# Performance work log

Measured on AMD Instinct MI355X. Metric: run time of the kernel, lower is better.

## Reference

```python
import jax, jax.numpy as jnp
import numpy as np

IN, H, B, T, OUT = 128, 512, 256, 512, 2

def _lstm_layer(x, Wih, Whh, bih, bhh):
    # x: [B, T, D_in] -> h_seq: [B, T, H]. PyTorch gate order: i, f, g, o.
    gx = jnp.einsum('btd,gd->btg', x, Wih) + bih + bhh  # [B, T, 4H]
    gx = jnp.transpose(gx, (1, 0, 2))                    # [T, B, 4H]
    Hh = Whh.shape[1]
    def step(carry, g_t):
        h, c = carry
        g = g_t + h @ Whh.T
        i = jax.nn.sigmoid(g[:, 0*Hh:1*Hh])
        f = jax.nn.sigmoid(g[:, 1*Hh:2*Hh])
        gg = jnp.tanh(g[:, 2*Hh:3*Hh])
        o = jax.nn.sigmoid(g[:, 3*Hh:4*Hh])
        c = f * c + i * gg
        h = o * jnp.tanh(c)
        return (h, c), h
    h0 = jnp.zeros((x.shape[0], Hh), x.dtype)
    (_, _), hs = jax.lax.scan(step, (h0, h0), gx)
    return jnp.transpose(hs, (1, 0, 2))  # [B, T, H]

def setup_inputs() -> dict:
    key = jax.random.key(0)
    ks = jax.random.split(key, 11)
    s = 1.0 / np.sqrt(H)
    u = lambda k, shp: jax.random.uniform(k, shp, jnp.float32, -s, s)
    return {
        'x':    jax.random.normal(ks[0], (B, T, IN), jnp.float32),
        'Wih0': u(ks[1], (4 * H, IN)), 'Whh0': u(ks[2], (4 * H, H)),
        'bih0': u(ks[3], (4 * H,)),    'bhh0': u(ks[4], (4 * H,)),
        'Wih1': u(ks[5], (4 * H, H)),  'Whh1': u(ks[6], (4 * H, H)),
        'bih1': u(ks[7], (4 * H,)),    'bhh1': u(ks[8], (4 * H,)),
        'Wfc':  u(ks[9], (OUT, H)),    'bfc':  u(ks[10], (OUT,)),
    }

def reference(x, Wih0, Whh0, bih0, bhh0, Wih1, Whh1, bih1, bhh1, Wfc, bfc):
    h1 = _lstm_layer(x, Wih0, Whh0, bih0, bhh0)   # layer 0
    h2 = _lstm_layer(h1, Wih1, Whh1, bih1, bhh1)  # layer 1
    return h2[:, -1, :] @ Wfc.T + bfc             # [B, OUT]
```

## Files before the change

### kernel.cpp

```cpp
#include <hip/hip_runtime.h>

#define IN_DIM 128
#define HID    512
#define BATCH  256
#define SEQT   512
#define G4H    2048
#define K0     640
#define K1     1024
#define NC0    20
#define NC1    32
#define ROWB   2048
#define FSTRIDE 32

typedef __attribute__((ext_vector_type(8))) short bf16x8;
typedef __attribute__((ext_vector_type(4))) float f32x4;

#define MFMA16 __builtin_amdgcn_mfma_f32_16x16x32_bf16
#define GL(r, g, c) ((r) * 132 + (g) * 33 + (c))

__device__ __forceinline__ unsigned short f2bf(float f) {
  unsigned u = __float_as_uint(f);
  u += 0x7fffu + ((u >> 16) & 1u);
  return (unsigned short)(u >> 16);
}
__device__ __forceinline__ float bf2f(unsigned short s) {
  return __uint_as_float(((unsigned)s) << 16);
}
__device__ __forceinline__ float sigm(float x) { return 1.0f / (1.0f + __expf(-x)); }
__device__ __forceinline__ float tanh_f(float x) {
  float xc = fminf(fmaxf(x, -15.0f), 15.0f);
  float e = __expf(2.0f * xc);
  return (e - 1.0f) / (e + 1.0f);
}

__device__ __forceinline__ unsigned ald(const unsigned* p) {
  return __hip_atomic_load(p, __ATOMIC_RELAXED, __HIP_MEMORY_SCOPE_AGENT);
}

__global__ void conv_weights(const float* __restrict__ Wih0, const float* __restrict__ Whh0,
                             const float* __restrict__ Wih1, const float* __restrict__ Whh1,
                             const float* __restrict__ bih0, const float* __restrict__ bhh0,
                             const float* __restrict__ bih1, const float* __restrict__ bhh1,
                             short* __restrict__ W0h, short* __restrict__ W0l,
                             short* __restrict__ W1h, short* __restrict__ W1l,
                             float* __restrict__ bsum0, float* __restrict__ bsum1) {
  int idx = blockIdx.x * blockDim.x + threadIdx.x;
  const int N0 = G4H * K0, N1 = G4H * K1;
  if (idx < N0) {
    int tile = idx / (K0 * 16), rem = idx % (K0 * 16);
    int kcg = rem >> 9, l = (rem >> 3) & 63, j = rem & 7;
    int slice = tile >> 2, g = tile & 3;
    int c = l & 15, k = kcg * 32 + ((l >> 4) << 3) + j;
    int n = g * HID + slice * 16 + c;
    float w = (k < IN_DIM) ? Wih0[n * IN_DIM + k] : Whh0[n * HID + (k - IN_DIM)];
    unsigned short hi = f2bf(w);
    W0h[idx] = (short)hi;
    W0l[idx] = (short)f2bf(w - bf2f(hi));
  } else if (idx < N0 + N1) {
    int d = idx - N0;
    int tile = d / (K1 * 16), rem = d % (K1 * 16);
    int kcg = rem >> 9, l = (rem >> 3) & 63, j = rem & 7;
    int slice = tile >> 2, g = tile & 3;
    int c = l & 15, k = kcg * 32 + ((l >> 4) << 3) + j;
    int n = g * HID + slice * 16 + c;
    float w = (k < HID) ? Wih1[n * HID + k] : Whh1[n * HID + (k - HID)];
    unsigned short hi = f2bf(w);
    W1h[d] = (short)hi;
    W1l[d] = (short)f2bf(w - bf2f(hi));
  } else if (idx < N0 + N1 + G4H) {
    int n = idx - (N0 + N1);
    bsum0[n] = bih0[n] + bhh0[n];
  } else if (idx < N0 + N1 + 2 * G4H) {
    int n = idx - (N0 + N1 + G4H);
    bsum1[n] = bih1[n] + bhh1[n];
  }
}

#define PKH(a, b) ((unsigned)((a) & 0xffffu) | (((b) & 0xffffu) << 16))
#define PKL(a, b) (((a) >> 16) | ((b) & 0xffff0000u))

__device__ __forceinline__ void unpack16(char* bh, char* bl, int byte0, int rx,
                                         const uint4& v0, const uint4& v1,
                                         const uint4& v2, const uint4& v3) {
  int4 h0 = {(int)PKH(v0.x, v0.y), (int)PKH(v0.z, v0.w), (int)PKH(v1.x, v1.y), (int)PKH(v1.z, v1.w)};
  int4 h1 = {(int)PKH(v2.x, v2.y), (int)PKH(v2.z, v2.w), (int)PKH(v3.x, v3.y), (int)PKH(v3.z, v3.w)};
  int4 l0 = {(int)PKL(v0.x, v0.y), (int)PKL(v0.z, v0.w), (int)PKL(v1.x, v1.y), (int)PKL(v1.z, v1.w)};
  int4 l1 = {(int)PKL(v2.x, v2.y), (int)PKL(v2.z, v2.w), (int)PKL(v3.x, v3.y), (int)PKL(v3.z, v3.w)};
  *(int4*)(bh + (byte0 ^ rx)) = h0;
  *(int4*)(bh + ((byte0 + 16) ^ rx)) = h1;
  *(int4*)(bl + (byte0 ^ rx)) = l0;
  *(int4*)(bl + ((byte0 + 16) ^ rx)) = l1;
}

__device__ __forceinline__ void stage_one(char* AhiB, char* AloB,
                                          const unsigned* __restrict__ plane,
                                          int b0, int colOff, int tid) {
  const int row = tid >> 5, c32 = tid & 31;
  const unsigned* p = plane + (size_t)(b0 + row) * HID + c32 * 16;
  uint4 v0, v1, v2, v3;
  asm volatile(
      "global_load_dwordx4 %0, %4, off sc0 sc1\n\t"
      "global_load_dwordx4 %1, %4, off offset:16 sc0 sc1\n\t"
      "global_load_dwordx4 %2, %4, off offset:32 sc0 sc1\n\t"
      "global_load_dwordx4 %3, %4, off offset:48 sc0 sc1\n\t"
      "s_waitcnt vmcnt(0)"
      : "=&v"(v0), "=&v"(v1), "=&v"(v2), "=&v"(v3)
      : "v"(p)
      : "memory");
  const int rx = (row & 7) << 4;
  unpack16(AhiB + row * ROWB, AloB + row * ROWB, (colOff + c32 * 16) * 2, rx, v0, v1, v2, v3);
}

__device__ __forceinline__ void stage_two(char* AhiB, char* AloB,
                                          const unsigned* __restrict__ pA,
                                          const unsigned* __restrict__ pB,
                                          int b0, int tid) {
  const int row = tid >> 5, c32 = tid & 31;
  const unsigned* p0 = pA + (size_t)(b0 + row) * HID + c32 * 16;
  const unsigned* p2 = pB + (size_t)(b0 + row) * HID + c32 * 16;
  uint4 v0, v1, v2, v3, w0, w1, w2, w3;
  asm volatile(
      "global_load_dwordx4 %0, %8, off sc0 sc1\n\t"
      "global_load_dwordx4 %1, %8, off offset:16 sc0 sc1\n\t"
      "global_load_dwordx4 %2, %8, off offset:32 sc0 sc1\n\t"
      "global_load_dwordx4 %3, %8, off offset:48 sc0 sc1\n\t"
      "global_load_dwordx4 %4, %9, off sc0 sc1\n\t"
      "global_load_dwordx4 %5, %9, off offset:16 sc0 sc1\n\t"
      "global_load_dwordx4 %6, %9, off offset:32 sc0 sc1\n\t"
      "global_load_dwordx4 %7, %9, off offset:48 sc0 sc1\n\t"
      "s_waitcnt vmcnt(0)"
      : "=&v"(v0), "=&v"(v1), "=&v"(v2), "=&v"(v3),
        "=&v"(w0), "=&v"(w1), "=&v"(w2), "=&v"(w3)
      : "v"(p0), "v"(p2)
      : "memory");
  const int rx = (row & 7) << 4;
  char* bh = AhiB + row * ROWB;
  char* bl = AloB + row * ROWB;
  unpack16(bh, bl, (c32 * 16) * 2, rx, v0, v1, v2, v3);
  unpack16(bh, bl, (HID + c32 * 16) * 2, rx, w0, w1, w2, w3);
}
#undef PKH
#undef PKL

template <int NKC>
__device__ __forceinline__ void gemm32(const char* Ah, const char* Al,
                                       const short* __restrict__ Bh0, const short* __restrict__ Bl0,
                                       const short* __restrict__ Bh1, const short* __restrict__ Bl1,
                                       int lane, int aoff,
                                       f32x4& a00, f32x4& a01, f32x4& a10, f32x4& a11) {
  const int row = lane & 15;
  const int ko  = (lane >> 4) * 8;
  const int rx  = (row & 7) << 4;
  const char* pAh0 = Ah + row * ROWB;
  const char* pAh1 = Ah + (row + 16) * ROWB;
  const char* pAl0 = Al + row * ROWB;
  const char* pAl1 = Al + (row + 16) * ROWB;
#pragma unroll
  for (int kc = 0; kc < NKC; ++kc) {
    const int off = ((aoff + kc * 32 + ko) * 2) ^ rx;
    bf16x8 ah0 = *(const bf16x8*)(pAh0 + off);
    bf16x8 ah1 = *(const bf16x8*)(pAh1 + off);
    bf16x8 al0 = *(const bf16x8*)(pAl0 + off);
    bf16x8 al1 = *(const bf16x8*)(pAl1 + off);
    bf16x8 bh0 = *(const bf16x8*)(Bh0 + kc * 512 + lane * 8);
    bf16x8 bl0 = *(const bf16x8*)(Bl0 + kc * 512 + lane * 8);
    bf16x8 bh1 = *(const bf16x8*)(Bh1 + kc * 512 + lane * 8);
    bf16x8 bl1 = *(const bf16x8*)(Bl1 + kc * 512 + lane * 8);
    a00 = MFMA16(ah0, bh0, a00, 0, 0, 0);
    a01 = MFMA16(ah1, bh0, a01, 0, 0, 0);
    a00 = MFMA16(ah0, bl0, a00, 0, 0, 0);
    a01 = MFMA16(ah1, bl0, a01, 0, 0, 0);
    a00 = MFMA16(al0, bh0, a00, 0, 0, 0);
    a01 = MFMA16(al1, bh0, a01, 0, 0, 0);
    a10 = MFMA16(ah0, bh1, a10, 0, 0, 0);
    a11 = MFMA16(ah1, bh1, a11, 0, 0, 0);
    a10 = MFMA16(ah0, bl1, a10, 0, 0, 0);
    a11 = MFMA16(ah1, bl1, a11, 0, 0, 0);
    a10 = MFMA16(al0, bh1, a10, 0, 0, 0);
    a11 = MFMA16(al1, bh1, a11, 0, 0, 0);
  }
}

__device__ __forceinline__ void finq32(float* glf, int g, int lane,
                                       const f32x4& a00, const f32x4& a01,
                                       const f32x4& a10, const f32x4& a11) {
  const int col = lane & 15;
  const int r0  = (lane >> 4) * 4;
#pragma unroll
  for (int r = 0; r < 4; ++r) {
    atomicAdd(glf + GL(r0 + r, g, col), a00[r]);
    atomicAdd(glf + GL(16 + r0 + r, g, col), a01[r]);
    atomicAdd(glf + GL(r0 + r, g, col + 16), a10[r]);
    atomicAdd(glf + GL(16 + r0 + r, g, col + 16), a11[r]);
  }
}

__device__ __forceinline__ void group_barrier(unsigned* flags, unsigned target,
                                              int tid, int wid) {
  asm volatile("s_waitcnt vmcnt(0)" ::: "memory");
  __syncthreads();
  if (tid < 64) {
    if (tid == 0)
      __hip_atomic_store(flags + wid * FSTRIDE, target,
                         __ATOMIC_RELAXED, __HIP_MEMORY_SCOPE_AGENT);
    const int i = (tid & 31) * FSTRIDE;
    while (true) {
      unsigned v = ald(flags + i);
      if (__all((int)(v >= target))) break;
      __builtin_amdgcn_s_sleep(1);
    }
  }
  __syncthreads();
}

__global__ void __launch_bounds__(1024, 4) lstm_fused(
    const float* __restrict__ x,
    const float* __restrict__ Wfc, const float* __restrict__ bfc,
    const short* __restrict__ W0h, const short* __restrict__ W0l,
    const short* __restrict__ W1h, const short* __restrict__ W1l,
    const float* __restrict__ bsum0, const float* __restrict__ bsum1,
    unsigned* __restrict__ h0s, unsigned* __restrict__ h2s,
    unsigned* __restrict__ counters,
    float* __restrict__ out) {
  const int tid  = threadIdx.x;
  const int wv   = tid >> 6;
  const int lane = tid & 63;
  const int wid  = blockIdx.x & 31;
  const int grp  = blockIdx.x >> 5;
  const int role = wid >> 4;
  const int w16  = wid & 15;
  const int hid0 = w16 * 32;
  const int b0   = grp * 32;
  unsigned* flags = counters + grp * (32 * FSTRIDE);

  __shared__ __align__(16) char AhiB[32 * ROWB];
  __shared__ __align__(16) char AloB[32 * ROWB];
  __shared__ float glf[32 * 132];

  const int g  = wv & 3;
  const int kq = wv >> 2;
  const int t0 = (w16 * 2) * 4 + g, t1 = t0 + 4;
  const short *Bh0, *Bl0, *Bh1, *Bl1;
  int aoff;
  if (role == 0) {
    Bh0 = W0h + ((size_t)t0 * NC0 + (size_t)kq * 5) * 512;
    Bl0 = W0l + ((size_t)t0 * NC0 + (size_t)kq * 5) * 512;
    Bh1 = W0h + ((size_t)t1 * NC0 + (size_t)kq * 5) * 512;
    Bl1 = W0l + ((size_t)t1 * NC0 + (size_t)kq * 5) * 512;
    aoff = kq * 160;
  } else {
    Bh0 = W1h + ((size_t)t0 * NC1 + (size_t)kq * 8) * 512;
    Bl0 = W1l + ((size_t)t0 * NC1 + (size_t)kq * 8) * 512;
    Bh1 = W1h + ((size_t)t1 * NC1 + (size_t)kq * 8) * 512;
    Bl1 = W1l + ((size_t)t1 * NC1 + (size_t)kq * 8) * 512;
    aoff = kq * 256;
  }

  float c = 0.f;
  float bs[4];
  {
    const int n = hid0 + (tid & 31);
    const float* bsp = role ? bsum1 : bsum0;
#pragma unroll
    for (int q = 0; q < 4; ++q) bs[q] = bsp[q * HID + n];
  }
  for (int i = tid; i < 32 * 132; i += 1024) glf[i] = 0.f;

  const size_t PL = (size_t)BATCH * HID;

  for (int s = 0; s <= SEQT; ++s) {
    const int cur = s & 1, prv = cur ^ 1;
    unsigned* h0c = h0s + (size_t)cur * PL;
    const unsigned* h0p = h0s + (size_t)prv * PL;
    unsigned* h2c = h2s + (size_t)cur * PL;
    const unsigned* h2p = h2s + (size_t)prv * PL;
    const bool active = role ? (s > 0) : (s < SEQT);

    if (active) {
      if (role == 0) {
        {
          const int row = tid >> 5, t32 = tid & 31;
          const int rx = (row & 7) << 4;
          const float* xs = x + ((size_t)(b0 + row) * SEQT + s) * IN_DIM + t32 * 4;
          float4 xv = *(const float4*)xs;
          unsigned short h0v = f2bf(xv.x), h1v = f2bf(xv.y), h2v = f2bf(xv.z), h3v = f2bf(xv.w);
          uint2 hd = {(unsigned)h0v | ((unsigned)h1v << 16), (unsigned)h2v | ((unsigned)h3v << 16)};
          uint2 ld = {(unsigned)f2bf(xv.x - bf2f(h0v)) | ((unsigned)f2bf(xv.y - bf2f(h1v)) << 16),
                      (unsigned)f2bf(xv.z - bf2f(h2v)) | ((unsigned)f2bf(xv.w - bf2f(h3v)) << 16)};
          const int byte = (t32 * 8) ^ rx;
          *(uint2*)(AhiB + row * ROWB + byte) = hd;
          *(uint2*)(AloB + row * ROWB + byte) = ld;
        }
        stage_one(AhiB, AloB, h0p, b0, IN_DIM, tid);
      } else {
        stage_two(AhiB, AloB, h0p, h2p, b0, tid);
      }
    }
    __syncthreads();

    if (active) {
      f32x4 a00 = {0.f, 0.f, 0.f, 0.f}, a01 = {0.f, 0.f, 0.f, 0.f};
      f32x4 a10 = {0.f, 0.f, 0.f, 0.f}, a11 = {0.f, 0.f, 0.f, 0.f};
      if (role == 0)
        gemm32<5>(AhiB, AloB, Bh0, Bl0, Bh1, Bl1, lane, aoff, a00, a01, a10, a11);
      else
        gemm32<8>(AhiB, AloB, Bh0, Bl0, Bh1, Bl1, lane, aoff, a00, a01, a10, a11);
      finq32(glf, g, lane, a00, a01, a10, a11);
    }
    __syncthreads();

    if (active) {
      const int row = tid >> 5, col = tid & 31;
      float gi = glf[GL(row, 0, col)] + bs[0];
      float gf = glf[GL(row, 1, col)] + bs[1];
      float gg = glf[GL(row, 2, col)] + bs[2];
      float go = glf[GL(row, 3, col)] + bs[3];
      glf[GL(row, 0, col)] = 0.f; glf[GL(row, 1, col)] = 0.f;
      glf[GL(row, 2, col)] = 0.f; glf[GL(row, 3, col)] = 0.f;
      float i = sigm(gi), f = sigm(gf), gv = tanh_f(gg), o = sigm(go);
      float cc = f * c + i * gv;
      c = cc;
      float h = o * tanh_f(cc);
      unsigned short hh = f2bf(h);
      unsigned short hl = f2bf(h - bf2f(hh));
      unsigned pk = (unsigned)hh | ((unsigned)hl << 16);
      unsigned* hc = role ? h2c : h0c;
      __hip_atomic_store(hc + (size_t)(b0 + row) * HID + hid0 + col, pk,
                         __ATOMIC_RELAXED, __HIP_MEMORY_SCOPE_AGENT);
    }

    group_barrier(flags, (unsigned)(s + 1), tid, wid);
  }

  {
    const int p = tid >> 3, q = tid & 7;
    float acc = 0.f;
    if (wid == 0 && tid < 512) {
      const int b = b0 + (p >> 1), o = p & 1;
      const unsigned* sp = h2s + (size_t)b * HID + q * 64;
      const float* wf = Wfc + (size_t)o * HID + q * 64;
#pragma unroll 8
      for (int i = 0; i < 64; ++i) {
        unsigned u = ald(sp + i);
        acc += (bf2f((unsigned short)(u & 0xffff)) + bf2f((unsigned short)(u >> 16))) * wf[i];
      }
      glf[p * 8 + q] = acc;
    }
    __syncthreads();
    if (wid == 0 && tid < 512 && q == 0) {
      float t = 0.f;
#pragma unroll
      for (int i = 0; i < 8; ++i) t += glf[p * 8 + i];
      out[(b0 + (p >> 1)) * 2 + (p & 1)] = t + bfc[p & 1];
    }
  }
}

extern "C" void kernel_launch(void* const* d_in, const int* in_sizes, int n_in,
                              void* d_out, int out_size, void* d_ws, size_t ws_size,
                              hipStream_t stream) {
  const float* x    = (const float*)d_in[0];
  const float* Wih0 = (const float*)d_in[1];
  const float* Whh0 = (const float*)d_in[2];
  const float* bih0 = (const float*)d_in[3];
  const float* bhh0 = (const float*)d_in[4];
  const float* Wih1 = (const float*)d_in[5];
  const float* Whh1 = (const float*)d_in[6];
  const float* bih1 = (const float*)d_in[7];
  const float* bhh1 = (const float*)d_in[8];
  const float* Wfc  = (const float*)d_in[9];
  const float* bfc  = (const float*)d_in[10];
  float* out = (float*)d_out;

  short* W0h = (short*)d_ws;
  short* W0l = W0h + (size_t)G4H * K0;
  short* W1h = W0l + (size_t)G4H * K0;
  short* W1l = W1h + (size_t)G4H * K1;
  unsigned* h0s = (unsigned*)(W1l + (size_t)G4H * K1);
  unsigned* h2s = h0s + (size_t)2 * BATCH * HID;
  unsigned* counters = h2s + (size_t)2 * BATCH * HID;
  float* bsum0 = (float*)(counters + 8 * 32 * FSTRIDE);
  float* bsum1 = bsum0 + G4H;

  (void)hipMemsetAsync(h0s, 0,
                       (size_t)4 * BATCH * HID * sizeof(unsigned) +
                           (size_t)8 * 32 * FSTRIDE * sizeof(unsigned),
                       stream);

  const int total = G4H * K0 + G4H * K1 + 2 * G4H;
  conv_weights<<<(total + 255) / 256, 256, 0, stream>>>(
      Wih0, Whh0, Wih1, Whh1, bih0, bhh0, bih1, bhh1,
      W0h, W0l, W1h, W1l, bsum0, bsum1);

  void* args[] = {(void*)&x,    (void*)&Wfc,  (void*)&bfc,
                  (void*)&W0h,  (void*)&W0l,  (void*)&W1h, (void*)&W1l,
                  (void*)&bsum0, (void*)&bsum1,
                  (void*)&h0s,  (void*)&h2s,  (void*)&counters, (void*)&out};
  (void)hipLaunchCooperativeKernel((void*)lstm_fused, dim3(256), dim3(1024), args, 0,
                                   stream);
}
```

Measured before the change: 16.71 ms.

## Store LSTM hidden state as single bf16 and drop its low-part MFMAs

The hidden states exchanged between workgroups are now stored as one bf16 value instead of a packed hi/lo bf16 pair. This halves the global traffic for the hidden state and the LDS staging buffer, and removes the low-part A-operand MFMAs for the recurrent terms. Only the x input still gets hi/lo splitting, which is applied for the first IN_DIM columns of layer 0. The cost is lower precision in the recurrent matmuls, which could increase error over 512 timesteps.

```diff
diff --git a/kernel.cpp b/kernel.cpp
--- a/kernel.cpp
+++ b/kernel.cpp
@@ -76,92 +76,80 @@
   }
 }
 
-#define PKH(a, b) ((unsigned)((a) & 0xffffu) | (((b) & 0xffffu) << 16))
-#define PKL(a, b) (((a) >> 16) | ((b) & 0xffff0000u))
-
-__device__ __forceinline__ void unpack16(char* bh, char* bl, int byte0, int rx,
-                                         const uint4& v0, const uint4& v1,
-                                         const uint4& v2, const uint4& v3) {
-  int4 h0 = {(int)PKH(v0.x, v0.y), (int)PKH(v0.z, v0.w), (int)PKH(v1.x, v1.y), (int)PKH(v1.z, v1.w)};
-  int4 h1 = {(int)PKH(v2.x, v2.y), (int)PKH(v2.z, v2.w), (int)PKH(v3.x, v3.y), (int)PKH(v3.z, v3.w)};
-  int4 l0 = {(int)PKL(v0.x, v0.y), (int)PKL(v0.z, v0.w), (int)PKL(v1.x, v1.y), (int)PKL(v1.z, v1.w)};
-  int4 l1 = {(int)PKL(v2.x, v2.y), (int)PKL(v2.z, v2.w), (int)PKL(v3.x, v3.y), (int)PKL(v3.z, v3.w)};
-  *(int4*)(bh + (byte0 ^ rx)) = h0;
-  *(int4*)(bh + ((byte0 + 16) ^ rx)) = h1;
-  *(int4*)(bl + (byte0 ^ rx)) = l0;
-  *(int4*)(bl + ((byte0 + 16) ^ rx)) = l1;
-}
-
-__device__ __forceinline__ void stage_one(char* AhiB, char* AloB,
-                                          const unsigned* __restrict__ plane,
-                                          int b0, int colOff, int tid) {
+
+__device__ __forceinline__ void stage_l0(char* Ah, const float* __restrict__ x,
+                                         const unsigned short* __restrict__ h0p,
+                                         int b0, int s, int tid) {
   const int row = tid >> 5, c32 = tid & 31;
-  const unsigned* p = plane + (size_t)(b0 + row) * HID + c32 * 16;
-  uint4 v0, v1, v2, v3;
+  const int rx = (row & 7) << 4;
+  char* base = Ah + row * ROWB;
+  {
+    const float* xs = x + ((size_t)(b0 + row) * SEQT + s) * IN_DIM + c32 * 4;
+    float4 xv = *(const float4*)xs;
+    unsigned short h0 = f2bf(xv.x), h1 = f2bf(xv.y), h2 = f2bf(xv.z), h3 = f2bf(xv.w);
+    uint2 hd = {(unsigned)h0 | ((unsigned)h1 << 16), (unsigned)h2 | ((unsigned)h3 << 16)};
+    uint2 ld = {(unsigned)f2bf(xv.x - bf2f(h0)) | ((unsigned)f2bf(xv.y - bf2f(h1)) << 16),
+                (unsigned)f2bf(xv.z - bf2f(h2)) | ((unsigned)f2bf(xv.w - bf2f(h3)) << 16)};
+    *(uint2*)(base + ((c32 * 8) ^ rx)) = hd;
+    *(uint2*)(base + ((1280 + c32 * 8) ^ rx)) = ld;
+  }
+  {
+    const unsigned short* hp = h0p + (size_t)(b0 + row) * HID + c32 * 16;
+    uint4 v0, v1;
+    asm volatile(
+        "global_load_dwordx4 %0, %2, off sc0 sc1\n\t"
+        "global_load_dwordx4 %1, %2, off offset:16 sc0 sc1\n\t"
+        "s_waitcnt vmcnt(0)"
+        : "=&v"(v0), "=&v"(v1) : "v"(hp) : "memory");
+    const int byte0 = 256 + c32 * 32;
+    *(int4*)(base + (byte0 ^ rx)) = *(int4*)&v0;
+    *(int4*)(base + ((byte0 + 16) ^ rx)) = *(int4*)&v1;
+  }
+}
+
+__device__ __forceinline__ void stage_l1(char* Ah,
+                                         const unsigned short* __restrict__ h0p,
+                                         const unsigned short* __restrict__ h2p,
+                                         int b0, int tid) {
+  const int row = tid >> 5, c32 = tid & 31;
+  const int rx = (row & 7) << 4;
+  char* base = Ah + row * ROWB;
+  const unsigned short* p0 = h0p + (size_t)(b0 + row) * HID + c32 * 16;
+  const unsigned short* p2 = h2p + (size_t)(b0 + row) * HID + c32 * 16;
+  uint4 v0, v1, w0, w1;
   asm volatile(
       "global_load_dwordx4 %0, %4, off sc0 sc1\n\t"
       "global_load_dwordx4 %1, %4, off offset:16 sc0 sc1\n\t"
-      "global_load_dwordx4 %2, %4, off offset:32 sc0 sc1\n\t"
-      "global_load_dwordx4 %3, %4, off offset:48 sc0 sc1\n\t"
+      "global_load_dwordx4 %2, %5, off sc0 sc1\n\t"
+      "global_load_dwordx4 %3, %5, off offset:16 sc0 sc1\n\t"
       "s_waitcnt vmcnt(0)"
-      : "=&v"(v0), "=&v"(v1), "=&v"(v2), "=&v"(v3)
-      : "v"(p)
-      : "memory");
-  const int rx = (row & 7) << 4;
-  unpack16(AhiB + row * ROWB, AloB + row * ROWB, (colOff + c32 * 16) * 2, rx, v0, v1, v2, v3);
-}
-
-__device__ __forceinline__ void stage_two(char* AhiB, char* AloB,
-                                          const unsigned* __restrict__ pA,
-                                          const unsigned* __restrict__ pB,
-                                          int b0, int tid) {
-  const int row = tid >> 5, c32 = tid & 31;
-  const unsigned* p0 = pA + (size_t)(b0 + row) * HID + c32 * 16;
-  const unsigned* p2 = pB + (size_t)(b0 + row) * HID + c32 * 16;
-  uint4 v0, v1, v2, v3, w0, w1, w2, w3;
-  asm volatile(
-      "global_load_dwordx4 %0, %8, off sc0 sc1\n\t"
-      "global_load_dwordx4 %1, %8, off offset:16 sc0 sc1\n\t"
-      "global_load_dwordx4 %2, %8, off offset:32 sc0 sc1\n\t"
-      "global_load_dwordx4 %3, %8, off offset:48 sc0 sc1\n\t"
-      "global_load_dwordx4 %4, %9, off sc0 sc1\n\t"
-      "global_load_dwordx4 %5, %9, off offset:16 sc0 sc1\n\t"
-      "global_load_dwordx4 %6, %9, off offset:32 sc0 sc1\n\t"
-      "global_load_dwordx4 %7, %9, off offset:48 sc0 sc1\n\t"
-      "s_waitcnt vmcnt(0)"
-      : "=&v"(v0), "=&v"(v1), "=&v"(v2), "=&v"(v3),
-        "=&v"(w0), "=&v"(w1), "=&v"(w2), "=&v"(w3)
-      : "v"(p0), "v"(p2)
-      : "memory");
-  const int rx = (row & 7) << 4;
-  char* bh = AhiB + row * ROWB;
-  char* bl = AloB + row * ROWB;
-  unpack16(bh, bl, (c32 * 16) * 2, rx, v0, v1, v2, v3);
-  unpack16(bh, bl, (HID + c32 * 16) * 2, rx, w0, w1, w2, w3);
-}
-#undef PKH
-#undef PKL
+      : "=&v"(v0), "=&v"(v1), "=&v"(w0), "=&v"(w1)
+      : "v"(p0), "v"(p2) : "memory");
+  const int b0b = c32 * 32;
+  *(int4*)(base + (b0b ^ rx)) = *(int4*)&v0;
+  *(int4*)(base + ((b0b + 16) ^ rx)) = *(int4*)&v1;
+  const int b2b = 1024 + c32 * 32;
+  *(int4*)(base + (b2b ^ rx)) = *(int4*)&w0;
+  *(int4*)(base + ((b2b + 16) ^ rx)) = *(int4*)&w1;
+}
 
 template <int NKC>
-__device__ __forceinline__ void gemm32(const char* Ah, const char* Al,
-                                       const short* __restrict__ Bh0, const short* __restrict__ Bl0,
-                                       const short* __restrict__ Bh1, const short* __restrict__ Bl1,
-                                       int lane, int aoff,
-                                       f32x4& a00, f32x4& a01, f32x4& a10, f32x4& a11) {
+__device__ __forceinline__ void gemm_seq(const char* Ah, bool xlo,
+                                         const short* __restrict__ Bh0, const short* __restrict__ Bl0,
+                                         const short* __restrict__ Bh1, const short* __restrict__ Bl1,
+                                         int lane, int aoff,
+                                         f32x4& a00, f32x4& a01, f32x4& a10, f32x4& a11) {
   const int row = lane & 15;
   const int ko  = (lane >> 4) * 8;
   const int rx  = (row & 7) << 4;
-  const char* pAh0 = Ah + row * ROWB;
-  const char* pAh1 = Ah + (row + 16) * ROWB;
-  const char* pAl0 = Al + row * ROWB;
-  const char* pAl1 = Al + (row + 16) * ROWB;
+  const char* pA0 = Ah + row * ROWB;
+  const char* pA1 = Ah + (row + 16) * ROWB;
 #pragma unroll
   for (int kc = 0; kc < NKC; ++kc) {
-    const int off = ((aoff + kc * 32 + ko) * 2) ^ rx;
-    bf16x8 ah0 = *(const bf16x8*)(pAh0 + off);
-    bf16x8 ah1 = *(const bf16x8*)(pAh1 + off);
-    bf16x8 al0 = *(const bf16x8*)(pAl0 + off);
-    bf16x8 al1 = *(const bf16x8*)(pAl1 + off);
+    const int k = aoff + kc * 32;
+    const int off = ((k + ko) * 2) ^ rx;
+    bf16x8 ah0 = *(const bf16x8*)(pA0 + off);
+    bf16x8 ah1 = *(const bf16x8*)(pA1 + off);
     bf16x8 bh0 = *(const bf16x8*)(Bh0 + kc * 512 + lane * 8);
     bf16x8 bl0 = *(const bf16x8*)(Bl0 + kc * 512 + lane * 8);
     bf16x8 bh1 = *(const bf16x8*)(Bh1 + kc * 512 + lane * 8);
@@ -170,14 +158,19 @@
     a01 = MFMA16(ah1, bh0, a01, 0, 0, 0);
     a00 = MFMA16(ah0, bl0, a00, 0, 0, 0);
     a01 = MFMA16(ah1, bl0, a01, 0, 0, 0);
-    a00 = MFMA16(al0, bh0, a00, 0, 0, 0);
-    a01 = MFMA16(al1, bh0, a01, 0, 0, 0);
     a10 = MFMA16(ah0, bh1, a10, 0, 0, 0);
     a11 = MFMA16(ah1, bh1, a11, 0, 0, 0);
     a10 = MFMA16(ah0, bl1, a10, 0, 0, 0);
     a11 = MFMA16(ah1, bl1, a11, 0, 0, 0);
-    a10 = MFMA16(al0, bh1, a10, 0, 0, 0);
-    a11 = MFMA16(al1, bh1, a11, 0, 0, 0);
+    if (xlo && k < IN_DIM) {
+      const int offl = ((1280 + (k + ko) * 2)) ^ rx;
+      bf16x8 al0 = *(const bf16x8*)(pA0 + offl);
+      bf16x8 al1 = *(const bf16x8*)(pA1 + offl);
+      a00 = MFMA16(al0, bh0, a00, 0, 0, 0);
+      a01 = MFMA16(al1, bh0, a01, 0, 0, 0);
+      a10 = MFMA16(al0, bh1, a10, 0, 0, 0);
+      a11 = MFMA16(al1, bh1, a11, 0, 0, 0);
+    }
   }
 }
 
@@ -219,7 +212,7 @@
     const short* __restrict__ W0h, const short* __restrict__ W0l,
     const short* __restrict__ W1h, const short* __restrict__ W1l,
     const float* __restrict__ bsum0, const float* __restrict__ bsum1,
-    unsigned* __restrict__ h0s, unsigned* __restrict__ h2s,
+    unsigned short* __restrict__ h0s, unsigned short* __restrict__ h2s,
     unsigned* __restrict__ counters,
     float* __restrict__ out) {
   const int tid  = threadIdx.x;
@@ -233,8 +226,7 @@
   const int b0   = grp * 32;
   unsigned* flags = counters + grp * (32 * FSTRIDE);
 
-  __shared__ __align__(16) char AhiB[32 * ROWB];
-  __shared__ __align__(16) char AloB[32 * ROWB];
+  __shared__ __align__(16) char AhB[32 * ROWB];
   __shared__ float glf[32 * 132];
 
   const int g  = wv & 3;
@@ -270,31 +262,15 @@
 
   for (int s = 0; s <= SEQT; ++s) {
     const int cur = s & 1, prv = cur ^ 1;
-    unsigned* h0c = h0s + (size_t)cur * PL;
-    const unsigned* h0p = h0s + (size_t)prv * PL;
-    unsigned* h2c = h2s + (size_t)cur * PL;
-    const unsigned* h2p = h2s + (size_t)prv * PL;
+    unsigned short* h0c = h0s + (size_t)cur * PL;
+    const unsigned short* h0p = h0s + (size_t)prv * PL;
+    unsigned short* h2c = h2s + (size_t)cur * PL;
+    const unsigned short* h2p = h2s + (size_t)prv * PL;
     const bool active = role ? (s > 0) : (s < SEQT);
 
     if (active) {
-      if (role == 0) {
-        {
-          const int row = tid >> 5, t32 = tid & 31;
-          const int rx = (row & 7) << 4;
-          const float* xs = x + ((size_t)(b0 + row) * SEQT + s) * IN_DIM + t32 * 4;
-          float4 xv = *(const float4*)xs;
-          unsigned short h0v = f2bf(xv.x), h1v = f2bf(xv.y), h2v = f2bf(xv.z), h3v = f2bf(xv.w);
-          uint2 hd = {(unsigned)h0v | ((unsigned)h1v << 16), (unsigned)h2v | ((unsigned)h3v << 16)};
-          uint2 ld = {(unsigned)f2bf(xv.x - bf2f(h0v)) | ((unsigned)f2bf(xv.y - bf2f(h1v)) << 16),
-                      (unsigned)f2bf(xv.z - bf2f(h2v)) | ((unsigned)f2bf(xv.w - bf2f(h3v)) << 16)};
-          const int byte = (t32 * 8) ^ rx;
-          *(uint2*)(AhiB + row * ROWB + byte) = hd;
-          *(uint2*)(AloB + row * ROWB + byte) = ld;
-        }
-        stage_one(AhiB, AloB, h0p, b0, IN_DIM, tid);
-      } else {
-        stage_two(AhiB, AloB, h0p, h2p, b0, tid);
-      }
+      if (role == 0) stage_l0(AhB, x, h0p, b0, s, tid);
+      else           stage_l1(AhB, h0p, h2p, b0, tid);
     }
     __syncthreads();
 
@@ -302,9 +278,9 @@
       f32x4 a00 = {0.f, 0.f, 0.f, 0.f}, a01 = {0.f, 0.f, 0.f, 0.f};
       f32x4 a10 = {0.f, 0.f, 0.f, 0.f}, a11 = {0.f, 0.f, 0.f, 0.f};
       if (role == 0)
-        gemm32<5>(AhiB, AloB, Bh0, Bl0, Bh1, Bl1, lane, aoff, a00, a01, a10, a11);
+        gemm_seq<5>(AhB, true, Bh0, Bl0, Bh1, Bl1, lane, aoff, a00, a01, a10, a11);
       else
-        gemm32<8>(AhiB, AloB, Bh0, Bl0, Bh1, Bl1, lane, aoff, a00, a01, a10, a11);
+        gemm_seq<8>(AhB, false, Bh0, Bl0, Bh1, Bl1, lane, aoff, a00, a01, a10, a11);
       finq32(glf, g, lane, a00, a01, a10, a11);
     }
     __syncthreads();
@@ -321,11 +297,9 @@
       float cc = f * c + i * gv;
       c = cc;
       float h = o * tanh_f(cc);
-      unsigned short hh = f2bf(h);
-      unsigned short hl = f2bf(h - bf2f(hh));
-      unsigned pk = (unsigned)hh | ((unsigned)hl << 16);
-      unsigned* hc = role ? h2c : h0c;
-      __hip_atomic_store(hc + (size_t)(b0 + row) * HID + hid0 + col, pk,
+      unsigned short hv = f2bf(h);
+      unsigned short* hc = role ? h2c : h0c;
+      __hip_atomic_store(hc + (size_t)(b0 + row) * HID + hid0 + col, hv,
                          __ATOMIC_RELAXED, __HIP_MEMORY_SCOPE_AGENT);
     }
 
@@ -337,12 +311,13 @@
     float acc = 0.f;
     if (wid == 0 && tid < 512) {
       const int b = b0 + (p >> 1), o = p & 1;
-      const unsigned* sp = h2s + (size_t)b * HID + q * 64;
+      const unsigned* sp = (const unsigned*)(h2s + (size_t)b * HID) + q * 32;
       const float* wf = Wfc + (size_t)o * HID + q * 64;
 #pragma unroll 8
-      for (int i = 0; i < 64; ++i) {
+      for (int i = 0; i < 32; ++i) {
         unsigned u = ald(sp + i);
-        acc += (bf2f((unsigned short)(u & 0xffff)) + bf2f((unsigned short)(u >> 16))) * wf[i];
+        acc += bf2f((unsigned short)(u & 0xffff)) * wf[2 * i] +
+               bf2f((unsigned short)(u >> 16)) * wf[2 * i + 1];
       }
       glf[p * 8 + q] = acc;
     }
@@ -376,14 +351,14 @@
   short* W0l = W0h + (size_t)G4H * K0;
   short* W1h = W0l + (size_t)G4H * K0;
   short* W1l = W1h + (size_t)G4H * K1;
-  unsigned* h0s = (unsigned*)(W1l + (size_t)G4H * K1);
-  unsigned* h2s = h0s + (size_t)2 * BATCH * HID;
-  unsigned* counters = h2s + (size_t)2 * BATCH * HID;
+  unsigned short* h0s = (unsigned short*)(W1l + (size_t)G4H * K1);
+  unsigned short* h2s = h0s + (size_t)2 * BATCH * HID;
+  unsigned* counters = (unsigned*)(h2s + (size_t)2 * BATCH * HID);
   float* bsum0 = (float*)(counters + 8 * 32 * FSTRIDE);
   float* bsum1 = bsum0 + G4H;
 
   (void)hipMemsetAsync(h0s, 0,
-                       (size_t)4 * BATCH * HID * sizeof(unsigned) +
+                       (size_t)4 * BATCH * HID * sizeof(unsigned short) +
                            (size_t)8 * 32 * FSTRIDE * sizeof(unsigned),
                        stream);
 
```

Result: faster. 14.55 ms, median of 2 (-12.9%).
